# Kernel tuning notes

Hardware: AMD Instinct MI355X
Metric: run time of the kernel (lower is better)

The kernel has to match this reference:

```python
import jax, jax.numpy as jnp
import numpy as np

B, T, D_IN, D_OUT, N_HEAD = 2, 2048, 1024, 1024, 16
HEAD_DIM = D_OUT // N_HEAD


def setup_inputs() -> dict:
    key = jax.random.key(0)
    k1, k2, k3, k4 = jax.random.split(key, 4)
    s = 0.02  # init scale for weights
    return {
        "x": jax.random.normal(k1, (B, T, D_IN), jnp.float32),
        "Wq": jax.random.normal(k2, (D_OUT, D_IN), jnp.float32) * s,
        "Wk": jax.random.normal(k3, (D_OUT, D_IN), jnp.float32) * s,
        "Wv": jax.random.normal(k4, (D_OUT, D_IN), jnp.float32) * s,
    }


def reference(x, Wq, Wk, Wv):
    b, t, _ = x.shape
    h, hd = N_HEAD, HEAD_DIM
    # Linear projections (torch Linear: x @ W.T), split heads -> [b,h,t,hd]
    q = (x @ Wq.T).reshape(b, t, h, hd).transpose(0, 2, 1, 3)
    k = (x @ Wk.T).reshape(b, t, h, hd).transpose(0, 2, 1, 3)
    v = (x @ Wv.T).reshape(b, t, h, hd).transpose(0, 2, 1, 3)
    # raw scores [b,h,t,t], causal mask BEFORE scaling (as in source)
    omega = jnp.einsum("bhqd,bhkd->bhqk", q, k)
    causal = jnp.triu(jnp.ones((t, t), dtype=bool), k=1)
    omega = jnp.where(causal, -jnp.inf, omega)
    attw = jax.nn.softmax(omega / jnp.sqrt(jnp.asarray(hd, omega.dtype)), axis=-1)
    ctx = jnp.einsum("bhqk,bhkd->bhqd", attw, v)  # [b,h,t,hd]
    # Faithful to source: transpose(2,3) then view(B,T,d_out)
    out = jnp.swapaxes(ctx, 2, 3).reshape(b, t, D_OUT)
    return out
```

## Files before the change

### kernel.cpp

```cpp
#include <hip/hip_runtime.h>
#include <hip/hip_bf16.h>
#include <stdint.h>

typedef __attribute__((ext_vector_type(8))) short s16x8;
typedef __attribute__((ext_vector_type(4))) float f32x4;

#define T_   2048
#define NH   16
#define HD   64
#define DIN  1024
#define SCALE_LOG2 0.18033688011112042f

#define MFMA32(a, b, c) __builtin_amdgcn_mfma_f32_16x16x32_bf16(a, b, c, 0, 0, 0)

__device__ __forceinline__ unsigned short f2bf(float f) {
  union { float f; uint32_t u; } c; c.f = f;
  uint32_t u = c.u;
  return (unsigned short)((u + 0x7FFFu + ((u >> 16) & 1u)) >> 16);
}

__device__ __forceinline__ uint32_t pk_bf16(float a, float b) {
  __hip_bfloat162 h = __float22bfloat162_rn(make_float2(a, b));
  return *reinterpret_cast<uint32_t*>(&h);
}

#define GLL(gp, lp) __builtin_amdgcn_global_load_lds( \
    (__attribute__((address_space(1))) void*)(gp),    \
    (__attribute__((address_space(3))) void*)(lp), 16, 0, 0)

__global__ __launch_bounds__(256) void cvt_kernel(
    const float* __restrict__ x,  const float* __restrict__ wq,
    const float* __restrict__ wk, const float* __restrict__ wv,
    unsigned short* __restrict__ xb, unsigned short* __restrict__ wb) {
  int i = (blockIdx.x * 256 + threadIdx.x) * 4;
  float4 v;
  unsigned short* dp;
  if (i < 4194304) {
    v = *(const float4*)(x + i);
    dp = xb + i;
  } else {
    int j = i - 4194304;
    int seg = j >> 20, r = j & 1048575;
    const float* w = (seg == 0) ? wq : (seg == 1) ? wk : wv;
    v = *(const float4*)(w + r);
    dp = wb + j;
  }
  ushort4 o;
  o.x = f2bf(v.x); o.y = f2bf(v.y); o.z = f2bf(v.z); o.w = f2bf(v.w);
  *(ushort4*)dp = o;
}

__global__ __launch_bounds__(256) void qkv_gemm(
    const unsigned short* __restrict__ A, const unsigned short* __restrict__ Bm,
    unsigned short* __restrict__ qkv) {
  __shared__ __attribute__((aligned(16))) unsigned short Alds[64 * 64];
  __shared__ __attribute__((aligned(16))) unsigned short Blds[128 * 64];
  const int tid = threadIdx.x;
  const int lane = tid & 63, wave = tid >> 6;
  const int wm = wave >> 1, wn = wave & 1;
  const int m0 = blockIdx.y * 64, n0 = blockIdx.x * 128;

  f32x4 acc[2][4] = {};

  const int srA = wave * 16 + (lane >> 3);
  const int srB = wave * 32 + (lane >> 3);
  const int scol = (((lane & 7) ^ ((lane >> 3) & 7))) * 8;
  const unsigned short* ag = A  + (size_t)(m0 + srA) * DIN + scol;
  const unsigned short* bg = Bm + (size_t)(n0 + srB) * DIN + scol;
  unsigned short* al = &Alds[wave * 16 * 64];
  unsigned short* bl = &Blds[wave * 32 * 64];

  const int l16 = lane & 15, quad = lane >> 4;
  const int sw = l16 & 7;

  for (int k0 = 0; k0 < DIN; k0 += 64) {
    __syncthreads();
#pragma unroll
    for (int i = 0; i < 2; i++)
      GLL(ag + (size_t)i * 8 * DIN + k0, al + i * 512);
#pragma unroll
    for (int i = 0; i < 4; i++)
      GLL(bg + (size_t)i * 8 * DIN + k0, bl + i * 512);
    __syncthreads();
#pragma unroll
    for (int ks = 0; ks < 2; ks++) {
      const int cl = ((ks * 4 + quad) ^ sw) * 8;
      s16x8 af[2], bf[4];
#pragma unroll
      for (int mt = 0; mt < 2; mt++)
        af[mt] = *(const s16x8*)&Alds[(wm * 32 + mt * 16 + l16) * 64 + cl];
#pragma unroll
      for (int nt = 0; nt < 4; nt++)
        bf[nt] = *(const s16x8*)&Blds[(wn * 64 + nt * 16 + l16) * 64 + cl];
#pragma unroll
      for (int mt = 0; mt < 2; mt++)
#pragma unroll
        for (int nt = 0; nt < 4; nt++)
          acc[mt][nt] = MFMA32(af[mt], bf[nt], acc[mt][nt]);
    }
  }

#pragma unroll
  for (int mt = 0; mt < 2; mt++) {
    int mbase = m0 + wm * 32 + mt * 16 + (quad << 2);
    int b = mbase >> 11, t = mbase & 2047;
#pragma unroll
    for (int nt = 0; nt < 4; nt++) {
      int n = n0 + wn * 64 + nt * 16 + l16;
      int sel = n >> 10, h = (n >> 6) & 15, d = n & 63;
      int bh = b * NH + h;
      if (sel == 2) {
        ushort4 pk;
        pk.x = f2bf(acc[mt][nt][0]); pk.y = f2bf(acc[mt][nt][1]);
        pk.z = f2bf(acc[mt][nt][2]); pk.w = f2bf(acc[mt][nt][3]);
        *(ushort4*)&qkv[8388608 + (size_t)(bh * HD + d) * T_ + t] = pk;
      } else {
        float qs = (sel == 0) ? SCALE_LOG2 : 1.f;
#pragma unroll
        for (int r = 0; r < 4; r++)
          qkv[(size_t)sel * 4194304 + (size_t)(bh * T_ + t + r) * HD + d] =
              f2bf(acc[mt][nt][r] * qs);
      }
    }
  }
}

__global__ __launch_bounds__(128) void attn_kernel(
    const unsigned short* __restrict__ qkv, float* __restrict__ out) {
  __shared__ __attribute__((aligned(16))) unsigned short Klds[2][64 * 64];
  __shared__ __attribute__((aligned(16))) unsigned short Vt[2][64 * 64];
  __shared__ __attribute__((aligned(16))) unsigned short Plds[64 * 64];

  const int lane = threadIdx.x & 63, wave = threadIdx.x >> 6;
  const int l16 = lane & 15, quad = lane >> 4;
  const int swl = l16 & 7;
  const int qt = 31 - blockIdx.y, bh = blockIdx.x;
  const int q0 = qt * 64;
  const size_t bh_off = (size_t)bh * (T_ * HD);
  const unsigned short* Q  = qkv + bh_off;
  const unsigned short* Kb = qkv + 4194304 + bh_off;
  const unsigned short* Vb = qkv + 8388608 + bh_off;

  s16x8 qf[2][2];
#pragma unroll
  for (int nt = 0; nt < 2; nt++) {
    const unsigned short* qp =
        Q + (size_t)(q0 + wave * 32 + nt * 16 + l16) * HD + quad * 8;
    qf[nt][0] = *(const s16x8*)(qp);
    qf[nt][1] = *(const s16x8*)(qp + 32);
  }

  const int r8 = lane >> 3;
  const int xc = ((lane & 7) ^ r8) * 8;
  const unsigned short* kg = Kb + (size_t)(wave * 32 + r8) * HD + xc;
  const unsigned short* vg = Vb + (size_t)(wave * 32 + r8) * T_ + xc;
  const int sbase = wave * 32 * 64;

  const s16x8 onesf = {0x3F80, 0x3F80, 0x3F80, 0x3F80,
                       0x3F80, 0x3F80, 0x3F80, 0x3F80};
  f32x4 o[2][4] = {};
  f32x4 lacc[2] = {};

#pragma unroll
  for (int i = 0; i < 4; i++) {
    GLL(kg + (size_t)i * 8 * HD, &Klds[0][sbase + i * 8 * 64]);
    GLL(vg + (size_t)i * 8 * T_, &Vt[0][sbase + i * 8 * 64]);
  }

  int cur = 0;
  for (int kt = 0; kt <= qt; kt++) {
    __syncthreads();
    if (kt < qt) {
      const unsigned short* kp = kg + (size_t)(kt + 1) * 64 * HD;
      const unsigned short* vp = vg + (kt + 1) * 64;
      unsigned short* kd = &Klds[cur ^ 1][sbase];
      unsigned short* vd = &Vt[cur ^ 1][sbase];
#pragma unroll
      for (int i = 0; i < 4; i++) {
        GLL(kp + (size_t)i * 8 * HD, kd + i * 8 * 64);
        GLL(vp + (size_t)i * 8 * T_, vd + i * 8 * 64);
      }
    }

    f32x4 s[4][2] = {};
#pragma unroll
    for (int kk = 0; kk < 2; kk++) {
      const int cl = ((kk * 4 + quad) ^ swl) * 8;
#pragma unroll
      for (int mt = 0; mt < 4; mt++) {
        s16x8 kf = *(const s16x8*)&Klds[cur][(mt * 16 + l16) * 64 + cl];
#pragma unroll
        for (int nt = 0; nt < 2; nt++)
          s[mt][nt] = MFMA32(kf, qf[nt][kk], s[mt][nt]);
      }
    }

    if (kt < qt) {
#pragma unroll
      for (int nt = 0; nt < 2; nt++) {
        uint32_t* prow = (uint32_t*)&Plds[(wave * 32 + nt * 16 + l16) * 64];
#pragma unroll
        for (int mt = 0; mt < 4; mt++) {
          float p0 = exp2f(s[mt][nt][0]);
          float p1 = exp2f(s[mt][nt][1]);
          float p2 = exp2f(s[mt][nt][2]);
          float p3 = exp2f(s[mt][nt][3]);
          *(uint2*)&prow[(((2 * mt + (quad >> 1)) ^ swl) << 2) +
                         (quad & 1) * 2] =
              make_uint2(pk_bf16(p0, p1), pk_bf16(p2, p3));
        }
      }
    } else {
#pragma unroll
      for (int nt = 0; nt < 2; nt++) {
        const int lim = wave * 32 + nt * 16 + l16;
        uint32_t* prow = (uint32_t*)&Plds[(wave * 32 + nt * 16 + l16) * 64];
#pragma unroll
        for (int mt = 0; mt < 4; mt++) {
          const int kb = mt * 16 + quad * 4;
          float p0 = (kb + 0 <= lim) ? exp2f(s[mt][nt][0]) : 0.f;
          float p1 = (kb + 1 <= lim) ? exp2f(s[mt][nt][1]) : 0.f;
          float p2 = (kb + 2 <= lim) ? exp2f(s[mt][nt][2]) : 0.f;
          float p3 = (kb + 3 <= lim) ? exp2f(s[mt][nt][3]) : 0.f;
          *(uint2*)&prow[(((2 * mt + (quad >> 1)) ^ swl) << 2) +
                         (quad & 1) * 2] =
              make_uint2(pk_bf16(p0, p1), pk_bf16(p2, p3));
        }
      }
    }

#pragma unroll
    for (int kk = 0; kk < 2; kk++) {
      const int cl = ((kk * 4 + quad) ^ swl) * 8;
      s16x8 pf[2];
#pragma unroll
      for (int nt = 0; nt < 2; nt++) {
        pf[nt] =
            *(const s16x8*)&Plds[(wave * 32 + nt * 16 + l16) * 64 + cl];
        lacc[nt] = MFMA32(pf[nt], onesf, lacc[nt]);
      }
#pragma unroll
      for (int dt = 0; dt < 4; dt++) {
        s16x8 vf = *(const s16x8*)&Vt[cur][(dt * 16 + l16) * 64 + cl];
#pragma unroll
        for (int nt = 0; nt < 2; nt++)
          o[nt][dt] = MFMA32(pf[nt], vf, o[nt][dt]);
      }
    }
    cur ^= 1;
  }

#pragma unroll
  for (int nt = 0; nt < 2; nt++) {
    f32x4 inv;
#pragma unroll
    for (int r = 0; r < 4; r++) inv[r] = 1.f / lacc[nt][r];
#pragma unroll
    for (int dt = 0; dt < 4; dt++) {
      float4 v = make_float4(o[nt][dt][0] * inv[0], o[nt][dt][1] * inv[1],
                             o[nt][dt][2] * inv[2], o[nt][dt][3] * inv[3]);
      *(float4*)(out + (size_t)bh * (HD * T_) + (size_t)(dt * 16 + l16) * T_ +
                 q0 + wave * 32 + nt * 16 + quad * 4) = v;
    }
  }
}

extern "C" void kernel_launch(void* const* d_in, const int* in_sizes, int n_in,
                              void* d_out, int out_size, void* d_ws, size_t ws_size,
                              hipStream_t stream) {
  const float* x  = (const float*)d_in[0];
  const float* wq = (const float*)d_in[1];
  const float* wk = (const float*)d_in[2];
  const float* wv = (const float*)d_in[3];
  float* out = (float*)d_out;

  unsigned short* xb  = (unsigned short*)d_ws;
  unsigned short* wb  = xb + 4194304;
  unsigned short* qkv = wb + 3145728;

  cvt_kernel<<<7168, 256, 0, stream>>>(x, wq, wk, wv, xb, wb);
  dim3 g1(24, 64);
  qkv_gemm<<<g1, 256, 0, stream>>>(xb, wb, qkv);
  dim3 g2(32, 32);
  attn_kernel<<<g2, 128, 0, stream>>>(qkv, out);
}
```

Before: 166.5 us.

## Split attention KV range across blocks with 128-row Q tiles and combine kernel

Attention now uses 128-query tiles with 4 waves per block, and the causal KV range of longer tiles is split into chunks of up to 8 key tiles. Each chunk runs in its own block, and a lookup table balances the work across 40 blocks per head. Split chunks write unnormalized partial outputs and row sums to workspace, and a new combine kernel sums them and normalizes. The async global-to-LDS double buffering is replaced by a register-staged single buffer with two barriers per iteration. This adds a kernel launch and extra memory traffic for the partials.

```diff
diff --git a/kernel.cpp b/kernel.cpp
--- a/kernel.cpp
+++ b/kernel.cpp
@@ -125,21 +125,37 @@
   }
 }
 
-__global__ __launch_bounds__(128) void attn_kernel(
-    const unsigned short* __restrict__ qkv, float* __restrict__ out) {
-  __shared__ __attribute__((aligned(16))) unsigned short Klds[2][64 * 64];
-  __shared__ __attribute__((aligned(16))) unsigned short Vt[2][64 * 64];
-  __shared__ __attribute__((aligned(16))) unsigned short Plds[64 * 64];
-
-  const int lane = threadIdx.x & 63, wave = threadIdx.x >> 6;
+__global__ __launch_bounds__(256) void attn_kernel(
+    const unsigned short* __restrict__ qkv, float* __restrict__ out,
+    float* __restrict__ op, float* __restrict__ lp) {
+  __shared__ __attribute__((aligned(16))) unsigned short Klds[64 * 64];
+  __shared__ __attribute__((aligned(16))) unsigned short Vt[64 * 64];
+  __shared__ __attribute__((aligned(16))) unsigned short Plds[128 * 64];
+
+  const int tid = threadIdx.x;
+  const int lane = tid & 63, wave = tid >> 6;
   const int l16 = lane & 15, quad = lane >> 4;
   const int swl = l16 & 7;
-  const int qt = 31 - blockIdx.y, bh = blockIdx.x;
-  const int q0 = qt * 64;
+  const int bh = blockIdx.x;
+
+  static const unsigned char QTt[40] = {
+      3, 4, 5, 6, 7, 7, 8, 8, 9, 9, 10, 10, 11, 11, 11, 12, 12, 12,
+      13, 13, 13, 14, 14, 14, 15, 15, 15, 15,
+      2, 6, 10, 14, 1, 5, 9, 13, 0, 4, 8, 12};
+  static const unsigned char CCt[40] = {
+      0, 0, 0, 0, 0, 1, 0, 1, 0, 1, 0, 1, 0, 1, 2, 0, 1, 2,
+      0, 1, 2, 0, 1, 2, 0, 1, 2, 3,
+      0, 1, 2, 3, 0, 1, 2, 3, 0, 1, 2, 3};
+  const int qt = QTt[blockIdx.y], c = CCt[blockIdx.y];
+  const int kt0 = c * 8;
+  const int kt1 = min(kt0 + 7, 2 * qt + 1);
+  const bool split = (qt >= 4);
+
   const size_t bh_off = (size_t)bh * (T_ * HD);
   const unsigned short* Q  = qkv + bh_off;
   const unsigned short* Kb = qkv + 4194304 + bh_off;
   const unsigned short* Vb = qkv + 8388608 + bh_off;
+  const int q0 = qt * 128;
 
   s16x8 qf[2][2];
 #pragma unroll
@@ -150,37 +166,35 @@
     qf[nt][1] = *(const s16x8*)(qp + 32);
   }
 
-  const int r8 = lane >> 3;
-  const int xc = ((lane & 7) ^ r8) * 8;
-  const unsigned short* kg = Kb + (size_t)(wave * 32 + r8) * HD + xc;
-  const unsigned short* vg = Vb + (size_t)(wave * 32 + r8) * T_ + xc;
-  const int sbase = wave * 32 * 64;
+  const int sr = tid >> 3;
+  const int sc = (tid & 7) * 8;
+  const int swc = (((tid & 7) ^ (sr & 7))) * 8;
+
+  s16x8 kr0 = *(const s16x8*)&Kb[(size_t)(kt0 * 64 + sr) * HD + sc];
+  s16x8 kr1 = *(const s16x8*)&Kb[(size_t)(kt0 * 64 + sr + 32) * HD + sc];
+  s16x8 vr0 = *(const s16x8*)&Vb[(size_t)sr * T_ + kt0 * 64 + sc];
+  s16x8 vr1 = *(const s16x8*)&Vb[(size_t)(sr + 32) * T_ + kt0 * 64 + sc];
 
   const s16x8 onesf = {0x3F80, 0x3F80, 0x3F80, 0x3F80,
                        0x3F80, 0x3F80, 0x3F80, 0x3F80};
   f32x4 o[2][4] = {};
   f32x4 lacc[2] = {};
 
-#pragma unroll
-  for (int i = 0; i < 4; i++) {
-    GLL(kg + (size_t)i * 8 * HD, &Klds[0][sbase + i * 8 * 64]);
-    GLL(vg + (size_t)i * 8 * T_, &Vt[0][sbase + i * 8 * 64]);
-  }
-
-  int cur = 0;
-  for (int kt = 0; kt <= qt; kt++) {
+  for (int kt = kt0; kt <= kt1; kt++) {
     __syncthreads();
-    if (kt < qt) {
-      const unsigned short* kp = kg + (size_t)(kt + 1) * 64 * HD;
-      const unsigned short* vp = vg + (kt + 1) * 64;
-      unsigned short* kd = &Klds[cur ^ 1][sbase];
-      unsigned short* vd = &Vt[cur ^ 1][sbase];
-#pragma unroll
-      for (int i = 0; i < 4; i++) {
-        GLL(kp + (size_t)i * 8 * HD, kd + i * 8 * 64);
-        GLL(vp + (size_t)i * 8 * T_, vd + i * 8 * 64);
-      }
-    }
+    *(s16x8*)&Klds[sr * 64 + swc] = kr0;
+    *(s16x8*)&Klds[(sr + 32) * 64 + swc] = kr1;
+    *(s16x8*)&Vt[sr * 64 + swc] = vr0;
+    *(s16x8*)&Vt[(sr + 32) * 64 + swc] = vr1;
+    if (kt < kt1) {
+      const unsigned short* kp = Kb + (size_t)(kt + 1) * 64 * HD;
+      const unsigned short* vp = Vb + (kt + 1) * 64;
+      kr0 = *(const s16x8*)&kp[(size_t)sr * HD + sc];
+      kr1 = *(const s16x8*)&kp[(size_t)(sr + 32) * HD + sc];
+      vr0 = *(const s16x8*)&vp[(size_t)sr * T_ + sc];
+      vr1 = *(const s16x8*)&vp[(size_t)(sr + 32) * T_ + sc];
+    }
+    __syncthreads();
 
     f32x4 s[4][2] = {};
 #pragma unroll
@@ -188,14 +202,14 @@
       const int cl = ((kk * 4 + quad) ^ swl) * 8;
 #pragma unroll
       for (int mt = 0; mt < 4; mt++) {
-        s16x8 kf = *(const s16x8*)&Klds[cur][(mt * 16 + l16) * 64 + cl];
+        s16x8 kf = *(const s16x8*)&Klds[(mt * 16 + l16) * 64 + cl];
 #pragma unroll
         for (int nt = 0; nt < 2; nt++)
           s[mt][nt] = MFMA32(kf, qf[nt][kk], s[mt][nt]);
       }
     }
 
-    if (kt < qt) {
+    if (kt < 2 * qt) {
 #pragma unroll
       for (int nt = 0; nt < 2; nt++) {
         uint32_t* prow = (uint32_t*)&Plds[(wave * 32 + nt * 16 + l16) * 64];
@@ -211,9 +225,10 @@
         }
       }
     } else {
+      const int dsh = (kt - 2 * qt) * 64;
 #pragma unroll
       for (int nt = 0; nt < 2; nt++) {
-        const int lim = wave * 32 + nt * 16 + l16;
+        const int lim = wave * 32 + nt * 16 + l16 - dsh;
         uint32_t* prow = (uint32_t*)&Plds[(wave * 32 + nt * 16 + l16) * 64];
 #pragma unroll
         for (int mt = 0; mt < 4; mt++) {
@@ -241,27 +256,73 @@
       }
 #pragma unroll
       for (int dt = 0; dt < 4; dt++) {
-        s16x8 vf = *(const s16x8*)&Vt[cur][(dt * 16 + l16) * 64 + cl];
+        s16x8 vf = *(const s16x8*)&Vt[(dt * 16 + l16) * 64 + cl];
 #pragma unroll
         for (int nt = 0; nt < 2; nt++)
           o[nt][dt] = MFMA32(pf[nt], vf, o[nt][dt]);
       }
     }
-    cur ^= 1;
-  }
-
-#pragma unroll
-  for (int nt = 0; nt < 2; nt++) {
-    f32x4 inv;
-#pragma unroll
-    for (int r = 0; r < 4; r++) inv[r] = 1.f / lacc[nt][r];
-#pragma unroll
-    for (int dt = 0; dt < 4; dt++) {
-      float4 v = make_float4(o[nt][dt][0] * inv[0], o[nt][dt][1] * inv[1],
-                             o[nt][dt][2] * inv[2], o[nt][dt][3] * inv[3]);
-      *(float4*)(out + (size_t)bh * (HD * T_) + (size_t)(dt * 16 + l16) * T_ +
-                 q0 + wave * 32 + nt * 16 + quad * 4) = v;
-    }
+  }
+
+  if (!split) {
+#pragma unroll
+    for (int nt = 0; nt < 2; nt++) {
+      f32x4 inv;
+#pragma unroll
+      for (int r = 0; r < 4; r++) inv[r] = 1.f / lacc[nt][r];
+#pragma unroll
+      for (int dt = 0; dt < 4; dt++) {
+        float4 v = make_float4(o[nt][dt][0] * inv[0], o[nt][dt][1] * inv[1],
+                               o[nt][dt][2] * inv[2], o[nt][dt][3] * inv[3]);
+        *(float4*)(out + (size_t)bh * (HD * T_) +
+                   (size_t)(dt * 16 + l16) * T_ + q0 + wave * 32 + nt * 16 +
+                   quad * 4) = v;
+      }
+    }
+  } else {
+    const int so = (qt < 8) ? (qt - 4) * 2
+                            : (qt < 12) ? 8 + (qt - 8) * 3 : 20 + (qt - 12) * 4;
+    const int slot = bh * 36 + so + c;
+    float* Op = op + (size_t)slot * 8192;
+    float* Lp = lp + (size_t)slot * 128;
+#pragma unroll
+    for (int nt = 0; nt < 2; nt++) {
+      const int qoff = wave * 32 + nt * 16 + quad * 4;
+#pragma unroll
+      for (int dt = 0; dt < 4; dt++) {
+        float4 v = make_float4(o[nt][dt][0], o[nt][dt][1], o[nt][dt][2],
+                               o[nt][dt][3]);
+        *(float4*)(Op + (dt * 16 + l16) * 128 + qoff) = v;
+      }
+      if (l16 == 0) {
+#pragma unroll
+        for (int r = 0; r < 4; r++) Lp[qoff + r] = lacc[nt][r];
+      }
+    }
+  }
+}
+
+__global__ __launch_bounds__(256) void combine_kernel(
+    const float* __restrict__ op, const float* __restrict__ lp,
+    float* __restrict__ out) {
+  const int bh = blockIdx.x, qt = blockIdx.y + 4;
+  const int nc = (2 * qt + 9) >> 3;
+  const int so = (qt < 8) ? (qt - 4) * 2
+                          : (qt < 12) ? 8 + (qt - 8) * 3 : 20 + (qt - 12) * 4;
+  const int base = bh * 36 + so;
+  const float* Op = op + (size_t)base * 8192;
+  const float* Lp = lp + (size_t)base * 128;
+  const int t = threadIdx.x;
+  const int q = t & 127, dg = t >> 7;
+  float lsum = 0.f;
+  for (int ci = 0; ci < nc; ci++) lsum += Lp[ci * 128 + q];
+  const float inv = 1.f / lsum;
+  float* ob = out + (size_t)bh * (HD * T_) + (size_t)qt * 128 + q;
+  for (int dd = 0; dd < 32; dd++) {
+    const int d = dg * 32 + dd;
+    float acc = 0.f;
+    for (int ci = 0; ci < nc; ci++) acc += Op[ci * 8192 + d * 128 + q];
+    ob[(size_t)d * T_] = acc * inv;
   }
 }
 
@@ -277,10 +338,14 @@
   unsigned short* xb  = (unsigned short*)d_ws;
   unsigned short* wb  = xb + 4194304;
   unsigned short* qkv = wb + 3145728;
+  float* op = (float*)(qkv + 12582912);
+  float* lp = op + 9437184;
 
   cvt_kernel<<<7168, 256, 0, stream>>>(x, wq, wk, wv, xb, wb);
   dim3 g1(24, 64);
   qkv_gemm<<<g1, 256, 0, stream>>>(xb, wb, qkv);
-  dim3 g2(32, 32);
-  attn_kernel<<<g2, 128, 0, stream>>>(qkv, out);
-}
+  dim3 g2(32, 40);
+  attn_kernel<<<g2, 256, 0, stream>>>(qkv, out, op, lp);
+  dim3 g3(32, 12);
+  combine_kernel<<<g3, 256, 0, stream>>>(op, lp, out);
+}
```

Result: slower. 187.3 us (+12.5%).
